# Performance work log

Hardware: AMD Instinct MI355X
Metric: run time of the kernel (lower is better)

## Reference

```python
import jax, jax.numpy as jnp
import numpy as np

B, K, DIM = 65536, 512, 128
EPS = 1e-8
LN_2PI = 1.83787706641


def setup_inputs() -> dict:
    key = jax.random.key(0)
    k1, k2, k3 = jax.random.split(key, 3)
    x = jax.random.normal(k1, (B, DIM), dtype=jnp.float32)
    centers = jax.random.uniform(k2, (K, DIM), dtype=jnp.float32)
    # torch init: 0.2 * rand + 0.9
    D_param = 0.2 * jax.random.uniform(k3, (K, DIM), dtype=jnp.float32) + 0.9
    return {"x": x, "centers": centers, "D_param": D_param}


def reference(x, centers, D_param):
    Bc, dim = x.shape
    Kc = centers.shape[0]
    Dabs = jnp.abs(D_param) + EPS          # [K, D]
    Dinv = 1.0 / Dabs                       # diagonal Sigma^{-1}
    log_det = jnp.sum(jnp.log(Dabs), axis=1)  # [K]
    dsf = -0.5 * log_det
    det_scale_safe = jnp.exp(dsf - jnp.max(dsf))  # [K]

    # dist_sq[b,k] = sum_d (x[b,d]-c[k,d])^2 * Dinv[k,d], via GEMM expansion
    # (avoids the [B,K,D] diff tensor the torch loop materializes)
    dist_sq = ((x * x) @ Dinv.T
               - 2.0 * (x @ (centers * Dinv).T)
               + jnp.sum(centers * centers * Dinv, axis=1)[None, :])  # [B, K]

    expo_gmm = -0.5 * dist_sq
    expo_cmm = jnp.power(dist_sq + 1.0, -((1.0 + dim) / 2.0))

    def log_resp(expo):
        safe = expo - jnp.max(expo, axis=-1, keepdims=True)
        numer = det_scale_safe[None, :] * jnp.exp(safe)
        denom = jnp.sum(numer, axis=1, keepdims=True)
        return jnp.log(jnp.clip(numer / denom, 1e-8))

    resp_gmm = log_resp(expo_gmm)
    resp_cmm = log_resp(expo_cmm)

    assign = jnp.argmax(resp_gmm, axis=1)                    # [B]
    onehot = jax.nn.one_hot(assign, Kc, dtype=expo_gmm.dtype)  # [B, K]
    ce = -0.5 * dim * LN_2PI + log_det[None, :] + expo_gmm
    # torch multiplies onehot twice; onehot^2 == onehot
    ce = (-1.0 / Bc) * jnp.sum(onehot * ce)

    # return_gmm and return_cmm both True
    a = jax.nn.softmax(resp_gmm, axis=-1)
    b = jax.nn.softmax(resp_cmm, axis=-1)
    resp = jnp.log((a + b) / 2.0)
    return resp, ce
```

## Files before the change

kernel.cpp:

```cpp
#include <hip/hip_runtime.h>
#include <math.h>

#define NROWS 65536
#define KCL   512
#define NDIM  128
#define CE_IDX ((size_t)NROWS * (size_t)KCL)
#define LN_2PI 1.83787706641f

using f32x4  = __attribute__((ext_vector_type(4))) float;
using short8 = __attribute__((ext_vector_type(8))) short;

__device__ __forceinline__ unsigned short f2bf(float f) {
    unsigned u = __float_as_uint(f);
    return (unsigned short)((u + 0x7fffu + ((u >> 16) & 1u)) >> 16);
}

__device__ __forceinline__ unsigned cvt_pk_bf16(float lo, float hi) {
    unsigned r;
    asm("v_cvt_pk_bf16_f32 %0, %1, %2" : "=v"(r) : "v"(lo), "v"(hi));
    return r;
}

__device__ __forceinline__ void gld_lds16(const void* g, void* l) {
    __builtin_amdgcn_global_load_lds(
        (const __attribute__((address_space(1))) unsigned int*)g,
        (__attribute__((address_space(3))) unsigned int*)l,
        16, 0, 0);
}

__global__ void k_prep(const float* __restrict__ centers,
                       const float* __restrict__ Dp,
                       unsigned short* __restrict__ W,
                       float* __restrict__ log_det,
                       float* __restrict__ cdotc) {
    int n = blockIdx.x;
    int d = threadIdx.x;
    int t = n >> 4, m = n & 15;
    float Dabs = fabsf(Dp[n * NDIM + d]) + 1e-8f;
    float dinv = 1.0f / Dabs;
    float c = centers[n * NDIM + d];
    int j1 = d, j2 = 128 + d;
    W[t * 4096 + (j1 >> 3) * 128 + m * 8 + (j1 & 7)] = f2bf(-2.0f * c * dinv);
    W[t * 4096 + (j2 >> 3) * 128 + m * 8 + (j2 & 7)] = f2bf(dinv);
    float lg = logf(Dabs);
    float cc = c * c * dinv;
    #pragma unroll
    for (int s = 32; s >= 1; s >>= 1) {
        lg += __shfl_xor(lg, s);
        cc += __shfl_xor(cc, s);
    }
    __shared__ float sred[4];
    if ((d & 63) == 0) { sred[(d >> 6) * 2 + 0] = lg; sred[(d >> 6) * 2 + 1] = cc; }
    __syncthreads();
    if (d == 0) { log_det[n] = sred[0] + sred[2]; cdotc[n] = sred[1] + sred[3]; }
}

__global__ __launch_bounds__(512) __attribute__((amdgpu_waves_per_eu(4, 8)))
void k_main(const float* __restrict__ x,
            const unsigned short* __restrict__ W,
            const float* __restrict__ log_det,
            const float* __restrict__ cdotc,
            float* __restrict__ out) {
    __shared__ __align__(16) short ldsW[3][8192];
    __shared__ float s_cd[KCL], s_ld[KCL], s_ds[KCL];
    __shared__ float ex_mn[2][64], ex_key[2][64], ex_ds[2][64], ex_sg[2][64];
    __shared__ float sred[8], ce_part[4];
    __shared__ float s_invsum;

    const int tid = threadIdx.x;
    {
        float ldv = log_det[tid];
        float cdv = cdotc[tid];
        s_ld[tid] = ldv;
        s_cd[tid] = cdv;
        float e = __expf(-0.5f * ldv);
        s_ds[tid] = e;
        float s = e;
        #pragma unroll
        for (int sh = 32; sh >= 1; sh >>= 1) s += __shfl_xor(s, sh);
        if ((tid & 63) == 0) sred[tid >> 6] = s;
    }

    const int lane = tid & 63;
    const int w = __builtin_amdgcn_readfirstlane(tid >> 6);
    const int g = w >> 1;
    const int h = w & 1;
    const int m = lane & 15;
    const int q = lane >> 4;
    const int r0 = blockIdx.x * 64;

    const float* xp = x + (size_t)(r0 + g * 16 + m) * NDIM + q * 8;
    short8 afx[4], afxx[4];
    #pragma unroll
    for (int kk = 0; kk < 4; kk++) {
        float4 a0 = *(const float4*)(xp + kk * 32);
        float4 a1 = *(const float4*)(xp + kk * 32 + 4);
        union { unsigned u[4]; short8 s; } A, AX;
        A.u[0]  = cvt_pk_bf16(a0.x, a0.y);
        A.u[1]  = cvt_pk_bf16(a0.z, a0.w);
        A.u[2]  = cvt_pk_bf16(a1.x, a1.y);
        A.u[3]  = cvt_pk_bf16(a1.z, a1.w);
        AX.u[0] = cvt_pk_bf16(a0.x * a0.x, a0.y * a0.y);
        AX.u[1] = cvt_pk_bf16(a0.z * a0.z, a0.w * a0.w);
        AX.u[2] = cvt_pk_bf16(a1.x * a1.x, a1.y * a1.y);
        AX.u[3] = cvt_pk_bf16(a1.z * a1.z, a1.w * a1.w);
        afx[kk] = A.s; afxx[kk] = AX.s;
    }

    f32x4 acc[16];
    #pragma unroll
    for (int t = 0; t < 16; t++) acc[t] = (f32x4){0.f, 0.f, 0.f, 0.f};

    const char* gWb = (const char*)W + ((w & 4) ? 16 * 8192 : 0)
                      + (w & 3) * 2048 + (size_t)lane * 16;
    char* lWb = (char*)&ldsW[0][0] + w * 2048;

    gld_lds16(gWb, lWb);
    gld_lds16(gWb + 1024, lWb + 1024);
    __syncthreads();

    if (tid == 0) {
        float tot = 0.0f;
        #pragma unroll
        for (int i = 0; i < 8; i++) tot += sred[i];
        s_invsum = 1.0f / tot;
    }

    #pragma unroll
    for (int u = 0; u < 16; ++u) {
        if (u < 15) {
            const char* s = gWb + (size_t)(u + 1) * 8192;
            char* l = (char*)&ldsW[0][0] + ((u + 1) % 3) * 16384 + w * 2048;
            gld_lds16(s, l);
            gld_lds16(s + 1024, l + 1024);
            asm volatile("s_waitcnt vmcnt(2)" ::: "memory");
        } else {
            asm volatile("s_waitcnt vmcnt(0)" ::: "memory");
        }
        __builtin_amdgcn_s_barrier();
        asm volatile("" ::: "memory");
        const short* lb = &ldsW[u % 3][h * 4096];
        #pragma unroll
        for (int kk = 0; kk < 4; kk++) {
            short8 b0 = *(const short8*)(lb + kk * 512 + lane * 8);
            short8 b1 = *(const short8*)(lb + 2048 + kk * 512 + lane * 8);
            acc[u] = __builtin_amdgcn_mfma_f32_16x16x32_bf16(afx[kk],  b0, acc[u], 0, 0, 0);
            acc[u] = __builtin_amdgcn_mfma_f32_16x16x32_bf16(afxx[kk], b1, acc[u], 0, 0, 0);
        }
    }

    const int colbase = h * 256 + m;
    float mn[4], bkey[4], bds[4];
    #pragma unroll
    for (int r = 0; r < 4; r++) { mn[r] = INFINITY; bkey[r] = INFINITY; bds[r] = 0.f; }
    #pragma unroll
    for (int u = 0; u < 16; u++) {
        const int col = colbase + u * 16;
        float cd = s_cd[col], ldc = s_ld[col];
        #pragma unroll
        for (int r = 0; r < 4; r++) {
            float ds = acc[u][r] + cd;
            acc[u][r] = ds;
            mn[r] = fminf(mn[r], ds);
            float key = ds + ldc;
            bool t = key < bkey[r];
            bkey[r] = t ? key : bkey[r];
            bds[r]  = t ? ds  : bds[r];
        }
    }
    #pragma unroll
    for (int s = 1; s < 16; s <<= 1) {
        #pragma unroll
        for (int r = 0; r < 4; r++) {
            mn[r] = fminf(mn[r], __shfl_xor(mn[r], s));
            float ok = __shfl_xor(bkey[r], s);
            float od = __shfl_xor(bds[r],  s);
            bool t = ok < bkey[r];
            bkey[r] = t ? ok : bkey[r];
            bds[r]  = t ? od : bds[r];
        }
    }
    const int rowb = g * 16 + q * 4;
    if (m == 0) {
        #pragma unroll
        for (int r = 0; r < 4; r++) {
            ex_mn[h][rowb + r]  = mn[r];
            ex_key[h][rowb + r] = bkey[r];
            ex_ds[h][rowb + r]  = bds[r];
        }
    }
    __syncthreads();

    float hmn[4], pay[4], Sg[4];
    #pragma unroll
    for (int r = 0; r < 4; r++) {
        mn[r] = fminf(mn[r], ex_mn[h ^ 1][rowb + r]);
        float ok = ex_key[h ^ 1][rowb + r];
        float od = ex_ds[h ^ 1][rowb + r];
        bool t = h ? (ok <= bkey[r]) : (ok < bkey[r]);
        float bk = t ? ok : bkey[r];
        float bd = t ? od : bds[r];
        pay[r] = fmaf(-1.5f, bd, bk);
        hmn[r] = 0.5f * mn[r];
        Sg[r] = 0.f;
    }

    #pragma unroll
    for (int u = 0; u < 16; u++) {
        float dsc = s_ds[colbase + u * 16];
        #pragma unroll
        for (int r = 0; r < 4; r++) {
            float ng = dsc * __expf(fmaf(-0.5f, acc[u][r], hmn[r]));
            Sg[r] += ng;
            acc[u][r] = ng;
        }
    }
    #pragma unroll
    for (int s = 1; s < 16; s <<= 1)
        #pragma unroll
        for (int r = 0; r < 4; r++) Sg[r] += __shfl_xor(Sg[r], s);

    if (m == 0) {
        #pragma unroll
        for (int r = 0; r < 4; r++) ex_sg[h][rowb + r] = Sg[r];
    }
    if (h == 0) {
        float ce = (pay[0] + pay[1]) + (pay[2] + pay[3]);
        if (m != 0) ce = 0.0f;
        ce += __shfl_xor(ce, 16);
        ce += __shfl_xor(ce, 32);
        if (lane == 0) ce_part[g] = ce;
    }
    __syncthreads();

    if (tid == 0) {
        float ce = (ce_part[0] + ce_part[1]) + (ce_part[2] + ce_part[3]);
        float v = (-1.0f / (float)NROWS) *
                  (ce + 64.0f * (-0.5f * (float)NDIM * LN_2PI));
        atomicAdd(out + CE_IDX, v);
    }

    float iSg05[4];
    #pragma unroll
    for (int r = 0; r < 4; r++)
        iSg05[r] = 0.5f / (Sg[r] + ex_sg[h ^ 1][rowb + r]);

    const float isum05 = 0.5f * s_invsum;
    #pragma unroll
    for (int u = 0; u < 16; u++) {
        float bt = s_ds[colbase + u * 16] * isum05;
        #pragma unroll
        for (int r = 0; r < 4; r++) {
            float z = fmaxf(acc[u][r] * iSg05[r], 5e-9f) + bt;
            out[(size_t)(r0 + g * 16 + q * 4 + r) * KCL + colbase + u * 16] = __logf(z);
        }
    }
}

extern "C" void kernel_launch(void* const* d_in, const int* in_sizes, int n_in,
                              void* d_out, int out_size, void* d_ws, size_t ws_size,
                              hipStream_t stream) {
    const float* x       = (const float*)d_in[0];
    const float* centers = (const float*)d_in[1];
    const float* Dp      = (const float*)d_in[2];
    float* out = (float*)d_out;

    unsigned short* W = (unsigned short*)d_ws;
    float* log_det = (float*)((char*)d_ws + (size_t)KCL * 256 * sizeof(unsigned short));
    float* cdotc   = log_det + KCL;

    k_prep<<<KCL, NDIM, 0, stream>>>(centers, Dp, W, log_det, cdotc);
    hipMemsetAsync(out + CE_IDX, 0, sizeof(float), stream);
    k_main<<<NROWS / 64, 512, 0, stream>>>(x, W, log_det, cdotc, out);
}
```

Measured before the change: 194.7 us.

## Deepen W prefetch to two stages, raise MFMA priority, fold memset into prep

The weight-tile pipeline now prefetches two tiles ahead into the triple LDS buffer, and its wait-and-barrier moves after the MFMA block so global-to-LDS loads overlap more compute. MFMA sections run under raised wave priority via s_setprio. The separate hipMemsetAsync that zeroes the CE accumulator is folded into the prep kernel to remove one launch. The barrier placement must still protect buffer reuse; with three buffers and a two-ahead prefetch, the ordering is tight.

```diff
diff --git a/kernel.cpp b/kernel.cpp
--- a/kernel.cpp
+++ b/kernel.cpp
@@ -32,7 +32,8 @@
                        const float* __restrict__ Dp,
                        unsigned short* __restrict__ W,
                        float* __restrict__ log_det,
-                       float* __restrict__ cdotc) {
+                       float* __restrict__ cdotc,
+                       float* __restrict__ ce_slot) {
     int n = blockIdx.x;
     int d = threadIdx.x;
     int t = n >> 4, m = n & 15;
@@ -52,7 +53,11 @@
     __shared__ float sred[4];
     if ((d & 63) == 0) { sred[(d >> 6) * 2 + 0] = lg; sred[(d >> 6) * 2 + 1] = cc; }
     __syncthreads();
-    if (d == 0) { log_det[n] = sred[0] + sred[2]; cdotc[n] = sred[1] + sred[3]; }
+    if (d == 0) {
+        log_det[n] = sred[0] + sred[2];
+        cdotc[n]   = sred[1] + sred[3];
+        if (n == 0) *ce_slot = 0.0f;
+    }
 }
 
 __global__ __launch_bounds__(512) __attribute__((amdgpu_waves_per_eu(4, 8)))
@@ -113,11 +118,15 @@
 
     const char* gWb = (const char*)W + ((w & 4) ? 16 * 8192 : 0)
                       + (w & 3) * 2048 + (size_t)lane * 16;
-    char* lWb = (char*)&ldsW[0][0] + w * 2048;
-
-    gld_lds16(gWb, lWb);
-    gld_lds16(gWb + 1024, lWb + 1024);
-    __syncthreads();
+    char* lW0 = (char*)&ldsW[0][0] + w * 2048;
+
+    gld_lds16(gWb, lW0);
+    gld_lds16(gWb + 1024, lW0 + 1024);
+    gld_lds16(gWb + 8192, lW0 + 16384);
+    gld_lds16(gWb + 8192 + 1024, lW0 + 16384 + 1024);
+    asm volatile("s_waitcnt vmcnt(2) lgkmcnt(0)" ::: "memory");
+    __builtin_amdgcn_s_barrier();
+    asm volatile("" ::: "memory");
 
     if (tid == 0) {
         float tot = 0.0f;
@@ -128,24 +137,30 @@
 
     #pragma unroll
     for (int u = 0; u < 16; ++u) {
-        if (u < 15) {
-            const char* s = gWb + (size_t)(u + 1) * 8192;
-            char* l = (char*)&ldsW[0][0] + ((u + 1) % 3) * 16384 + w * 2048;
+        if (u < 14) {
+            const char* s = gWb + (size_t)(u + 2) * 8192;
+            char* l = (char*)&ldsW[0][0] + ((u + 2) % 3) * 16384 + w * 2048;
             gld_lds16(s, l);
             gld_lds16(s + 1024, l + 1024);
-            asm volatile("s_waitcnt vmcnt(2)" ::: "memory");
-        } else {
-            asm volatile("s_waitcnt vmcnt(0)" ::: "memory");
-        }
-        __builtin_amdgcn_s_barrier();
-        asm volatile("" ::: "memory");
+        }
         const short* lb = &ldsW[u % 3][h * 4096];
+        __builtin_amdgcn_s_setprio(1);
         #pragma unroll
         for (int kk = 0; kk < 4; kk++) {
             short8 b0 = *(const short8*)(lb + kk * 512 + lane * 8);
             short8 b1 = *(const short8*)(lb + 2048 + kk * 512 + lane * 8);
             acc[u] = __builtin_amdgcn_mfma_f32_16x16x32_bf16(afx[kk],  b0, acc[u], 0, 0, 0);
             acc[u] = __builtin_amdgcn_mfma_f32_16x16x32_bf16(afxx[kk], b1, acc[u], 0, 0, 0);
+        }
+        __builtin_amdgcn_s_setprio(0);
+        if (u < 14) {
+            asm volatile("s_waitcnt vmcnt(2)" ::: "memory");
+        } else if (u == 14) {
+            asm volatile("s_waitcnt vmcnt(0)" ::: "memory");
+        }
+        if (u < 15) {
+            __builtin_amdgcn_s_barrier();
+            asm volatile("" ::: "memory");
         }
     }
 
@@ -269,7 +284,6 @@
     float* log_det = (float*)((char*)d_ws + (size_t)KCL * 256 * sizeof(unsigned short));
     float* cdotc   = log_det + KCL;
 
-    k_prep<<<KCL, NDIM, 0, stream>>>(centers, Dp, W, log_det, cdotc);
-    hipMemsetAsync(out + CE_IDX, 0, sizeof(float), stream);
+    k_prep<<<KCL, NDIM, 0, stream>>>(centers, Dp, W, log_det, cdotc, out + CE_IDX);
     k_main<<<NROWS / 64, 512, 0, stream>>>(x, W, log_det, cdotc, out);
 }
```

Result: no change. 196.3 us (+0.8%).
